# Optimization experiments

Measured on AMD Instinct MI355X. Metric: run time of the kernel, lower is better.

## Reference

```python
import jax, jax.numpy as jnp
import numpy as np

N = 100000   # nodes
E = 1600000  # edges (before self-loops)
HIDDEN = 256
BN_EPS = 1e-5


def setup_inputs() -> dict:
    key = jax.random.key(0)
    ks = jax.random.split(key, 16)
    def lin(k, i, o):
        return jax.random.normal(k, (i, o), jnp.float32) / np.float32(np.sqrt(i))
    inp = {
        "x": jax.random.normal(ks[0], (N, 21), jnp.float32),
        "edge_index": jax.random.randint(ks[1], (2, E), 0, N),
        # GCNConv weights (stored [in, out]) + biases
        "W1": lin(ks[2], 21, HIDDEN), "b1": jnp.zeros((HIDDEN,), jnp.float32),
        "W2": lin(ks[3], HIDDEN, 112), "b2": jnp.zeros((112,), jnp.float32),
        # dense MLP
        "lin2_w": lin(ks[4], 112, 256), "lin2_b": jnp.zeros((256,), jnp.float32),
        "lin3_w": lin(ks[5], 256, 100), "lin3_b": jnp.zeros((100,), jnp.float32),
        "lin4_w": lin(ks[6], 100, 1),   "lin4_b": jnp.zeros((1,), jnp.float32),
        # batchnorm affine params
        "g1": jnp.ones((112,), jnp.float32), "be1": jnp.zeros((112,), jnp.float32),
        "g2": jnp.ones((256,), jnp.float32), "be2": jnp.zeros((256,), jnp.float32),
        "g3": jnp.ones((100,), jnp.float32), "be3": jnp.zeros((100,), jnp.float32),
    }
    return inp


def _gcn_conv(x, W, b, src, dst, n):
    # PyG GCNConv: h = xW; out_i = sum_j norm_ij * h_j (+ bias), sym-normalized w/ self-loops
    h = x @ W                                              # [N, C]
    deg = jax.ops.segment_sum(jnp.ones(src.shape, h.dtype), dst, num_segments=n)
    dinv = jnp.where(deg > 0, jax.lax.rsqrt(deg), 0.0)
    norm = dinv[src] * dinv[dst]                            # [E']
    out = jax.ops.segment_sum(h[src] * norm[:, None], dst, num_segments=n)
    return out + b


def _bn(x, g, b):
    # train-mode batchnorm: biased batch variance
    m = jnp.mean(x, axis=0)
    v = jnp.mean(jnp.square(x - m), axis=0)
    return (x - m) * jax.lax.rsqrt(v + BN_EPS) * g + b


def reference(x, edge_index, W1, b1, W2, b2, lin2_w, lin2_b, lin3_w, lin3_b,
              lin4_w, lin4_b, g1, be1, g2, be2, g3, be3):
    n = x.shape[0]
    loops = jnp.arange(n, dtype=edge_index.dtype)
    src = jnp.concatenate([edge_index[0], loops])
    dst = jnp.concatenate([edge_index[1], loops])
    h = jax.nn.relu(_gcn_conv(x, W1, b1, src, dst, n))
    h = _gcn_conv(h, W2, b2, src, dst, n)
    h = jax.nn.relu(_bn(h, g1, be1))
    # dropout: identity (eval / deterministic)
    h = jax.nn.relu(_bn(h @ lin2_w + lin2_b, g2, be2))
    h = jax.nn.relu(_bn(h @ lin3_w + lin3_b, g3, be3))
    return h @ lin4_w + lin4_b
```

## Files before the change

kernel.cpp:

```cpp
#include <hip/hip_runtime.h>

#define N_NODES 100000
#define N_EDGES 1600000

typedef _Float16 f16x8 __attribute__((ext_vector_type(8)));
typedef _Float16 f16x4 __attribute__((ext_vector_type(4)));
typedef float fx4 __attribute__((ext_vector_type(4)));

#define NREP 16
#define NBUCK 196
#define CHUNK 8192
#define BCAP 12288

__global__ __launch_bounds__(256) void k_bin(const int* __restrict__ ei,
                                             unsigned* __restrict__ binned,
                                             int* __restrict__ gcount) {
  __shared__ unsigned pr[CHUNK];
  __shared__ unsigned srt[CHUNK];
  __shared__ unsigned char bk[CHUNK];
  __shared__ int hist[256], scanb[256], offs[256], bs[256], gb[256];
  const int t = threadIdx.x;
  const int e0 = blockIdx.x * CHUNK;
  const int n = min(CHUNK, N_EDGES - e0);
  hist[t] = 0;
  __syncthreads();
  for (int i = t; i < n; i += 256) {
    int src = ei[e0 + i], dst = ei[N_EDGES + e0 + i];
    int b = dst >> 9;
    pr[i] = ((unsigned)src << 9) | (unsigned)(dst & 511);
    bk[i] = (unsigned char)b;
    atomicAdd(&hist[b], 1);
  }
  __syncthreads();
  int v = hist[t];
  scanb[t] = v;
  __syncthreads();
  for (int off = 1; off < 256; off <<= 1) {
    int a = (t >= off) ? scanb[t - off] : 0;
    __syncthreads();
    scanb[t] += a;
    __syncthreads();
  }
  offs[t] = scanb[t] - v;
  bs[t] = scanb[t] - v;
  __syncthreads();
  for (int i = t; i < n; i += 256) {
    int b = bk[i];
    int p = atomicAdd(&offs[b], 1);
    srt[p] = pr[i];
  }
  if (t < NBUCK && v > 0) gb[t] = atomicAdd(&gcount[t], v);
  __syncthreads();
  int wave = t >> 6, lane = t & 63;
  for (int b = wave; b < NBUCK; b += 4) {
    int c = hist[b];
    if (c == 0) continue;
    int ls = bs[b], base = gb[b];
    unsigned* dstp = binned + (size_t)b * BCAP + base;
    for (int i = lane; i < c; i += 64) dstp[i] = srt[ls + i];
  }
}

__global__ void k_bscan(const int* __restrict__ gcount, int* __restrict__ gbase) {
  __shared__ int s[256];
  int t = threadIdx.x;
  int v = (t < NBUCK) ? gcount[t] : 0;
  s[t] = v;
  __syncthreads();
  for (int off = 1; off < 256; off <<= 1) {
    int a = (t >= off) ? s[t - off] : 0;
    __syncthreads();
    s[t] += a;
    __syncthreads();
  }
  if (t < NBUCK) gbase[t] = s[t] - v;
}

__global__ __launch_bounds__(256) void k_csr(const unsigned* __restrict__ binned,
                                             const int* __restrict__ gcount,
                                             const int* __restrict__ gbase,
                                             int* __restrict__ rowoff,
                                             int* __restrict__ cnt,
                                             float* __restrict__ dinv,
                                             int* __restrict__ csr) {
  __shared__ int hist[512], offs[512], ps[256];
  __shared__ unsigned srt[BCAP];
  const int b = blockIdx.x, t = threadIdx.x;
  const int n = min(gcount[b], BCAP);
  const int gb0 = gbase[b];
  const unsigned* bp = binned + (size_t)b * BCAP;
  hist[t] = 0;
  hist[t + 256] = 0;
  __syncthreads();
  for (int i = t; i < n; i += 256) atomicAdd(&hist[bp[i] & 511], 1);
  __syncthreads();
  int e0v = hist[2 * t], e1v = hist[2 * t + 1];
  ps[t] = e0v + e1v;
  __syncthreads();
  for (int off = 1; off < 256; off <<= 1) {
    int a = (t >= off) ? ps[t - off] : 0;
    __syncthreads();
    ps[t] += a;
    __syncthreads();
  }
  int excl = ps[t] - (e0v + e1v);
  offs[2 * t] = excl;
  offs[2 * t + 1] = excl + e0v;
  __syncthreads();
#pragma unroll
  for (int u = 0; u < 2; ++u) {
    int j = 2 * t + u;
    int nd = (b << 9) + j;
    if (nd < N_NODES) {
      int c = hist[j];
      cnt[nd] = c;
      dinv[nd] = rsqrtf((float)(c + 1));
      rowoff[nd] = gb0 + offs[j];
    }
  }
  __syncthreads();
  for (int i = t; i < n; i += 256) {
    unsigned p = bp[i];
    int d = p & 511;
    int pos = atomicAdd(&offs[d], 1);
    srt[pos] = p >> 9;
  }
  __syncthreads();
  for (int i = t; i < n; i += 256) csr[gb0 + i] = (int)srt[i];
}

__global__ void k_xpad(const float* __restrict__ x, const float* __restrict__ dinv,
                       _Float16* __restrict__ xs) {
  int idx = blockIdx.x * 256 + threadIdx.x;
  if (idx >= N_NODES * 24) return;
  int r = idx / 24, c = idx - r * 24;
  xs[idx] = (_Float16)((c < 21) ? x[r * 21 + c] * dinv[r] : 0.f);
}

__global__ __launch_bounds__(256) void k_aggx(
    const f16x8* __restrict__ xs3, const float* __restrict__ dinv,
    const int* __restrict__ rowoff, const int* __restrict__ cnt,
    const int* __restrict__ csr, float* __restrict__ aggx) {
  int lane = threadIdx.x & 63, wave = threadIdx.x >> 6;
  int j = lane / 3, c = lane - j * 3;
  if (j >= 21) return;
  int i = blockIdx.x * 84 + wave * 21 + j;
  if (i >= N_NODES) return;
  float di = dinv[i];
  int start = rowoff[i], len = cnt[i];
  f16x8 u = xs3[i * 3 + c];
  float a0[8], a1[8], a2[8], a3[8];
#pragma unroll
  for (int t = 0; t < 8; ++t) { a0[t] = (float)u[t]; a1[t] = a2[t] = a3[t] = 0.f; }
  int e = 0;
  for (; e + 3 < len; e += 4) {
    int s0 = csr[start + e], s1 = csr[start + e + 1];
    int s2 = csr[start + e + 2], s3 = csr[start + e + 3];
    f16x8 u0 = xs3[s0 * 3 + c];
    f16x8 u1 = xs3[s1 * 3 + c];
    f16x8 u2 = xs3[s2 * 3 + c];
    f16x8 u3 = xs3[s3 * 3 + c];
#pragma unroll
    for (int t = 0; t < 8; ++t) {
      a0[t] += (float)u0[t]; a1[t] += (float)u1[t];
      a2[t] += (float)u2[t]; a3[t] += (float)u3[t];
    }
  }
  for (; e < len; ++e) {
    int s0 = csr[start + e];
    f16x8 u0 = xs3[s0 * 3 + c];
#pragma unroll
    for (int t = 0; t < 8; ++t) a0[t] += (float)u0[t];
  }
  float4 r0, r1;
  r0.x = di * (a0[0] + a1[0] + a2[0] + a3[0]);
  r0.y = di * (a0[1] + a1[1] + a2[1] + a3[1]);
  r0.z = di * (a0[2] + a1[2] + a2[2] + a3[2]);
  r0.w = di * (a0[3] + a1[3] + a2[3] + a3[3]);
  r1.x = di * (a0[4] + a1[4] + a2[4] + a3[4]);
  r1.y = di * (a0[5] + a1[5] + a2[5] + a3[5]);
  r1.z = di * (a0[6] + a1[6] + a2[6] + a3[6]);
  r1.w = di * (a0[7] + a1[7] + a2[7] + a3[7]);
  *(float4*)(aggx + (size_t)i * 24 + c * 8) = r0;
  *(float4*)(aggx + (size_t)i * 24 + c * 8 + 4) = r1;
}

__global__ __launch_bounds__(256) void k_gemm1(const float4* __restrict__ aggx4,
                                               const float* __restrict__ W1,
                                               const float* __restrict__ b1,
                                               _Float16* __restrict__ h1) {
  __shared__ float As[32][24];
  int t = threadIdx.x;
  int base = blockIdx.x * 32;
  for (int idx = t; idx < 32 * 6; idx += 256) {
    int m = idx / 6, q = idx - m * 6;
    *(float4*)(&As[m][q * 4]) = aggx4[(base + m) * 6 + q];
  }
  float w[21];
#pragma unroll
  for (int k = 0; k < 21; ++k) w[k] = W1[k * 256 + t];
  float bias = b1[t];
  __syncthreads();
  for (int m = 0; m < 32; ++m) {
    float acc = bias;
#pragma unroll
    for (int k = 0; k < 21; ++k) acc = fmaf(As[m][k], w[k], acc);
    h1[(size_t)(base + m) * 256 + t] = (_Float16)fmaxf(acc, 0.f);
  }
}

template <int K, int KPAD, int NOUT, int NR>
__global__ void k_wcvt(const float* __restrict__ W, _Float16* __restrict__ Wh) {
  int idx = blockIdx.x * 256 + threadIdx.x;
  if (idx >= NR * KPAD) return;
  int n = idx / KPAD, k = idx % KPAD;
  float v = (n < NOUT && k < K) ? W[k * NOUT + n] : 0.f;
  Wh[idx] = (_Float16)v;
}

template <int K, int KPAD, int NT, int MT, int WR, int WC, int MINW,
          bool BN, bool STATS, bool F16IN, bool F16OUT>
__global__ __launch_bounds__(256, MINW) void k_mgemm(
    const void* __restrict__ Av, const _Float16* __restrict__ Wt,
    const float* __restrict__ bias, const float* __restrict__ bn_a,
    const float* __restrict__ bn_c, const float* __restrict__ rowscale,
    void* __restrict__ Cv, int NOUTr, float* __restrict__ sums,
    float* __restrict__ sqs) {
  constexpr int BM = WR * MT * 16;
  constexpr int NR = WC * NT * 16;
  constexpr int BKP = 40;
  constexpr int NC = KPAD / 32;
  constexpr int AIT = BM * 4 / 256;
  constexpr int ABYTES = BM * BKP * 2;
  constexpr int BBYTES = NR * BKP * 2;
  __shared__ __align__(16) char smem[ABYTES + BBYTES];
  _Float16* Ah = (_Float16*)smem;
  _Float16* Bh = (_Float16*)(smem + ABYTES);
  const float* A32 = (const float*)Av;
  const _Float16* A16 = (const _Float16*)Av;
  float* C = (float*)Cv;
  _Float16* C16 = (_Float16*)Cv;

  const int tid = threadIdx.x;
  const int lane = tid & 63, wave = tid >> 6;
  const int wr = wave % WR, wc = wave / WR;
  const int quad = lane >> 4, ln = lane & 15;
  const int rowbase = blockIdx.x * BM;

  fx4 acc[MT][NT];
#pragma unroll
  for (int mt = 0; mt < MT; ++mt)
#pragma unroll
    for (int j = 0; j < NT; ++j) acc[mt][j] = (fx4){0.f, 0.f, 0.f, 0.f};

  f16x8 pf16[AIT];
  fx4 pf32a[AIT], pf32b[AIT];

  auto loadA = [&](int kc) {
#pragma unroll
    for (int it = 0; it < AIT; ++it) {
      int idx = tid + it * 256;
      int m = idx >> 2, q = idx & 3;
      int gi = rowbase + m;
      int k = kc * 32 + q * 8;
      bool ok = (gi < N_NODES) && (k < K);
      if constexpr (F16IN) {
        f16x8 z;
#pragma unroll
        for (int t = 0; t < 8; ++t) z[t] = (_Float16)0;
        pf16[it] = ok ? *(const f16x8*)(A16 + (size_t)gi * K + k) : z;
      } else {
        if (ok) {
          pf32a[it] = *(const fx4*)(A32 + (size_t)gi * K + k);
          pf32b[it] = *(const fx4*)(A32 + (size_t)gi * K + k + 4);
        } else {
          pf32a[it] = (fx4){0.f, 0.f, 0.f, 0.f};
          pf32b[it] = (fx4){0.f, 0.f, 0.f, 0.f};
        }
      }
    }
  };

  auto writeA = [&](int kc) {
#pragma unroll
    for (int it = 0; it < AIT; ++it) {
      int idx = tid + it * 256;
      int m = idx >> 2, q = idx & 3;
      int k = kc * 32 + q * 8;
      float vv[8];
      if constexpr (F16IN) {
#pragma unroll
        for (int t = 0; t < 8; ++t) vv[t] = (float)pf16[it][t];
      } else {
#pragma unroll
        for (int t = 0; t < 4; ++t) { vv[t] = pf32a[it][t]; vv[t + 4] = pf32b[it][t]; }
      }
      if constexpr (BN) {
        if (k < K) {
          float4 a0 = *(const float4*)(bn_a + k);
          float4 a1 = *(const float4*)(bn_a + k + 4);
          float4 c0 = *(const float4*)(bn_c + k);
          float4 c1 = *(const float4*)(bn_c + k + 4);
          float av[8] = {a0.x, a0.y, a0.z, a0.w, a1.x, a1.y, a1.z, a1.w};
          float cv[8] = {c0.x, c0.y, c0.z, c0.w, c1.x, c1.y, c1.z, c1.w};
#pragma unroll
          for (int t = 0; t < 8; ++t) vv[t] = fmaxf(fmaf(vv[t], av[t], cv[t]), 0.f);
        }
      }
      f16x8 hv;
#pragma unroll
      for (int t = 0; t < 8; ++t) hv[t] = (_Float16)vv[t];
      *(f16x8*)(Ah + m * BKP + q * 8) = hv;
    }
  };

  loadA(0);
  for (int kc = 0; kc < NC; ++kc) {
    __syncthreads();
    writeA(kc);
    for (int idx = tid; idx < NR * 4; idx += 256) {
      int n = idx >> 2, p = idx & 3;
      *(f16x8*)(Bh + n * BKP + p * 8) =
          *(const f16x8*)(Wt + n * KPAD + kc * 32 + p * 8);
    }
    __syncthreads();
    if (kc + 1 < NC) loadA(kc + 1);
    f16x8 nf[MT];
#pragma unroll
    for (int mt = 0; mt < MT; ++mt) {
      int r = (wr * MT + mt) * 16 + ln;
      nf[mt] = *(const f16x8*)(Ah + r * BKP + quad * 8);
    }
#pragma unroll
    for (int j = 0; j < NT; ++j) {
      int n = (wc * NT + j) * 16 + ln;
      f16x8 wh = *(const f16x8*)(Bh + n * BKP + quad * 8);
#pragma unroll
      for (int mt = 0; mt < MT; ++mt)
        acc[mt][j] = __builtin_amdgcn_mfma_f32_16x16x32_f16(wh, nf[mt], acc[mt][j], 0, 0, 0);
    }
  }

  float* s_s = (float*)smem;
  float* s_q = s_s + NR;
  __syncthreads();
  if constexpr (STATS) {
    for (int c = tid; c < 2 * NR; c += 256) s_s[c] = 0.f;
    __syncthreads();
  }
  float rs[MT];
#pragma unroll
  for (int mt = 0; mt < MT; ++mt) {
    int nd = rowbase + (wr * MT + mt) * 16 + ln;
    rs[mt] = (rowscale != nullptr && nd < N_NODES) ? rowscale[nd] : 1.f;
  }
#pragma unroll
  for (int j = 0; j < NT; ++j) {
    int ch0 = (wc * NT + j) * 16 + quad * 4;
    bool cv = ch0 < NOUTr;
    float4 b4 = make_float4(0.f, 0.f, 0.f, 0.f);
    if (cv && bias != nullptr) b4 = *(const float4*)(bias + ch0);
    float sc[4] = {0.f, 0.f, 0.f, 0.f}, sq[4] = {0.f, 0.f, 0.f, 0.f};
#pragma unroll
    for (int mt = 0; mt < MT; ++mt) {
      int nd = rowbase + (wr * MT + mt) * 16 + ln;
      if (nd < N_NODES && cv) {
        float v0 = (acc[mt][j][0] + b4.x) * rs[mt];
        float v1 = (acc[mt][j][1] + b4.y) * rs[mt];
        float v2 = (acc[mt][j][2] + b4.z) * rs[mt];
        float v3 = (acc[mt][j][3] + b4.w) * rs[mt];
        if constexpr (F16OUT) {
          f16x4 o = {(_Float16)v0, (_Float16)v1, (_Float16)v2, (_Float16)v3};
          *(f16x4*)(C16 + (size_t)nd * NOUTr + ch0) = o;
        } else {
          float4 o = make_float4(v0, v1, v2, v3);
          *(float4*)(C + (size_t)nd * NOUTr + ch0) = o;
        }
        if constexpr (STATS) {
          sc[0] += v0; sq[0] = fmaf(v0, v0, sq[0]);
          sc[1] += v1; sq[1] = fmaf(v1, v1, sq[1]);
          sc[2] += v2; sq[2] = fmaf(v2, v2, sq[2]);
          sc[3] += v3; sq[3] = fmaf(v3, v3, sq[3]);
        }
      }
    }
    if constexpr (STATS) {
      if (cv) {
#pragma unroll
        for (int r = 0; r < 4; ++r) {
          float s = sc[r], q = sq[r];
          s += __shfl_xor(s, 1); q += __shfl_xor(q, 1);
          s += __shfl_xor(s, 2); q += __shfl_xor(q, 2);
          s += __shfl_xor(s, 4); q += __shfl_xor(q, 4);
          s += __shfl_xor(s, 8); q += __shfl_xor(q, 8);
          if (ln == 0) {
            atomicAdd(&s_s[ch0 + r], s);
            atomicAdd(&s_q[ch0 + r], q);
          }
        }
      }
    }
  }
  if constexpr (STATS) {
    __syncthreads();
    int rep = (blockIdx.x & (NREP - 1));
    for (int c = tid; c < NR; c += 256) {
      if (c < NOUTr) {
        atomicAdd(&sums[rep * NOUTr + c], s_s[c]);
        atomicAdd(&sqs[rep * NOUTr + c], s_q[c]);
      }
    }
  }
}

__global__ __launch_bounds__(256) void k_agg2(
    const f16x8* __restrict__ t2s8, const float* __restrict__ dinv,
    const int* __restrict__ rowoff, const int* __restrict__ cnt,
    const int* __restrict__ csr, const float* __restrict__ b2,
    _Float16* __restrict__ g2) {
  int lane = threadIdx.x & 63, wave = threadIdx.x >> 6;
  int j = lane / 14, c = lane - j * 14;
  if (j >= 4) return;
  int i = blockIdx.x * 16 + wave * 4 + j;
  float di = dinv[i];
  int start = rowoff[i], len = cnt[i];
  f16x8 u = t2s8[i * 14 + c];
  float a0[8], a1[8], a2[8], a3[8];
#pragma unroll
  for (int t = 0; t < 8; ++t) { a0[t] = (float)u[t]; a1[t] = a2[t] = a3[t] = 0.f; }
  int e = 0;
  for (; e + 3 < len; e += 4) {
    int s0 = csr[start + e], s1 = csr[start + e + 1];
    int s2 = csr[start + e + 2], s3 = csr[start + e + 3];
    f16x8 u0 = t2s8[s0 * 14 + c];
    f16x8 u1 = t2s8[s1 * 14 + c];
    f16x8 u2 = t2s8[s2 * 14 + c];
    f16x8 u3 = t2s8[s3 * 14 + c];
#pragma unroll
    for (int t = 0; t < 8; ++t) {
      a0[t] += (float)u0[t]; a1[t] += (float)u1[t];
      a2[t] += (float)u2[t]; a3[t] += (float)u3[t];
    }
  }
  for (; e < len; ++e) {
    int s0 = csr[start + e];
    f16x8 u0 = t2s8[s0 * 14 + c];
#pragma unroll
    for (int t = 0; t < 8; ++t) a0[t] += (float)u0[t];
  }
  float4 blo = *(const float4*)(b2 + c * 8);
  float4 bhi = *(const float4*)(b2 + c * 8 + 4);
  float bb[8] = {blo.x, blo.y, blo.z, blo.w, bhi.x, bhi.y, bhi.z, bhi.w};
  f16x8 o;
#pragma unroll
  for (int t = 0; t < 8; ++t)
    o[t] = (_Float16)fmaf(di, a0[t] + a1[t] + a2[t] + a3[t], bb[t]);
  *(f16x8*)(g2 + (size_t)i * 112 + c * 8) = o;
}

template <int C>
__global__ void k_colstats16(const _Float16* __restrict__ X, float* __restrict__ sums,
                             float* __restrict__ sqs) {
  int c = threadIdx.x;
  if (c >= C) return;
  int chunk = (N_NODES + gridDim.x - 1) / gridDim.x;
  int i0 = blockIdx.x * chunk;
  int i1 = min(N_NODES, i0 + chunk);
  float s = 0.f, q = 0.f;
  for (int i = i0; i < i1; ++i) {
    float v = (float)X[(size_t)i * C + c];
    s += v;
    q = fmaf(v, v, q);
  }
  int rep = (blockIdx.x & (NREP - 1));
  atomicAdd(&sums[rep * C + c], s);
  atomicAdd(&sqs[rep * C + c], q);
}

template <int C>
__global__ void k_bnfinal(const float* __restrict__ sums, const float* __restrict__ sqs,
                          const float* __restrict__ gamma, const float* __restrict__ beta,
                          float* __restrict__ bn_a, float* __restrict__ bn_c) {
  int c = threadIdx.x;
  if (c >= C) return;
  float s = 0.f, q = 0.f;
#pragma unroll
  for (int r = 0; r < NREP; ++r) {
    s += sums[r * C + c];
    q += sqs[r * C + c];
  }
  const float inv_n = 1.0f / (float)N_NODES;
  float mean = s * inv_n;
  float var = fmaxf(q * inv_n - mean * mean, 0.f);
  float rstd = 1.0f / sqrtf(var + 1e-5f);
  float a = gamma[c] * rstd;
  bn_a[c] = a;
  bn_c[c] = beta[c] - mean * a;
}

__global__ void k_final(const float* __restrict__ h4, const float* __restrict__ bn_a,
                        const float* __restrict__ bn_c, const float* __restrict__ w4,
                        const float* __restrict__ b4, float* __restrict__ out) {
  int lane = threadIdx.x & 63;
  int i = blockIdx.x * 4 + (threadIdx.x >> 6);
  float acc = fmaxf(fmaf(h4[(size_t)i * 100 + lane], bn_a[lane], bn_c[lane]), 0.f) * w4[lane];
  if (lane < 36) {
    int k = lane + 64;
    acc += fmaxf(fmaf(h4[(size_t)i * 100 + k], bn_a[k], bn_c[k]), 0.f) * w4[k];
  }
#pragma unroll
  for (int off = 32; off >= 1; off >>= 1) acc += __shfl_down(acc, off);
  if (lane == 0) out[i] = acc + b4[0];
}

extern "C" void kernel_launch(void* const* d_in, const int* in_sizes, int n_in,
                              void* d_out, int out_size, void* d_ws, size_t ws_size,
                              hipStream_t stream) {
  const float* x   = (const float*)d_in[0];
  const int*   ei  = (const int*)d_in[1];
  const float* W1  = (const float*)d_in[2];
  const float* b1  = (const float*)d_in[3];
  const float* W2  = (const float*)d_in[4];
  const float* b2  = (const float*)d_in[5];
  const float* l2w = (const float*)d_in[6];
  const float* l2b = (const float*)d_in[7];
  const float* l3w = (const float*)d_in[8];
  const float* l3b = (const float*)d_in[9];
  const float* l4w = (const float*)d_in[10];
  const float* l4b = (const float*)d_in[11];
  const float* g1  = (const float*)d_in[12];
  const float* be1 = (const float*)d_in[13];
  const float* g2w = (const float*)d_in[14];
  const float* be2 = (const float*)d_in[15];
  const float* g3  = (const float*)d_in[16];
  const float* be3 = (const float*)d_in[17];
  float* out = (float*)d_out;

  char* base = (char*)d_ws;
  size_t off = 0;
  auto alloc = [&](size_t bytes) -> char* {
    char* p = base + off;
    off = (off + bytes + 255) & ~(size_t)255;
    return p;
  };
  int*   cnt    = (int*)alloc((size_t)N_NODES * 4);
  int*   rowoff = (int*)alloc((size_t)N_NODES * 4);
  float* dinv   = (float*)alloc((size_t)N_NODES * 4);
  int*   csr    = (int*)alloc((size_t)N_EDGES * 4);
  unsigned* binned = (unsigned*)alloc((size_t)NBUCK * BCAP * 4);
  int*   gcount = (int*)alloc(NBUCK * 4);
  int*   gbase  = (int*)alloc(NBUCK * 4);
  float* stats  = (float*)alloc((size_t)NREP * 960 * 4);
  float* bnco   = (float*)alloc(960 * 4);
  _Float16* xs  = (_Float16*)alloc((size_t)N_NODES * 24 * 2);
  float* aggx   = (float*)alloc((size_t)N_NODES * 24 * 4);
  _Float16* h1  = (_Float16*)alloc((size_t)N_NODES * 256 * 2);
  _Float16* t2s = (_Float16*)alloc((size_t)N_NODES * 112 * 2);
  _Float16* g2h = (_Float16*)alloc((size_t)N_NODES * 112 * 2);
  float* h4     = (float*)alloc((size_t)N_NODES * 112 * 4);
  _Float16* wt2 = (_Float16*)alloc(112 * 256 * 2);
  _Float16* wt3 = (_Float16*)alloc(256 * 128 * 2);
  _Float16* wt4 = (_Float16*)alloc(112 * 256 * 2);

  float* sums1 = stats;
  float* sqs1  = sums1 + NREP * 112;
  float* sums2 = sqs1 + NREP * 112;
  float* sqs2  = sums2 + NREP * 256;
  float* sums3 = sqs2 + NREP * 256;
  float* sqs3  = sums3 + NREP * 112;
  float* bn_a1 = bnco + 0,   *bn_c1 = bnco + 112;
  float* bn_a2 = bnco + 224, *bn_c2 = bnco + 480;
  float* bn_a3 = bnco + 736, *bn_c3 = bnco + 848;

  hipMemsetAsync(gcount, 0, NBUCK * 4, stream);
  hipMemsetAsync(stats, 0, (size_t)NREP * 960 * 4, stream);

  k_bin<<<NBUCK, 256, 0, stream>>>(ei, binned, gcount);
  k_bscan<<<1, 256, 0, stream>>>(gcount, gbase);
  k_csr<<<NBUCK, 256, 0, stream>>>(binned, gcount, gbase, rowoff, cnt, dinv, csr);

  k_wcvt<256, 256, 112, 112><<<112, 256, 0, stream>>>(W2, wt2);
  k_wcvt<112, 128, 256, 256><<<128, 256, 0, stream>>>(l2w, wt3);
  k_wcvt<256, 256, 100, 112><<<112, 256, 0, stream>>>(l3w, wt4);

  k_xpad<<<(N_NODES * 24 + 255) / 256, 256, 0, stream>>>(x, dinv, xs);
  k_aggx<<<(N_NODES + 83) / 84, 256, 0, stream>>>((const f16x8*)xs, dinv, rowoff,
                                                  cnt, csr, aggx);
  k_gemm1<<<3125, 256, 0, stream>>>((const float4*)aggx, W1, b1, h1);

  k_mgemm<256, 256, 7, 2, 4, 1, 4, false, false, true, true><<<782, 256, 0, stream>>>(
      h1, wt2, nullptr, nullptr, nullptr, dinv, t2s, 112, nullptr, nullptr);
  k_agg2<<<6250, 256, 0, stream>>>((const f16x8*)t2s, dinv, rowoff, cnt, csr, b2,
                                   g2h);

  k_colstats16<112><<<1600, 128, 0, stream>>>(g2h, sums1, sqs1);
  k_bnfinal<112><<<1, 128, 0, stream>>>(sums1, sqs1, g1, be1, bn_a1, bn_c1);

  k_mgemm<112, 128, 8, 2, 2, 2, 4, true, true, true, true><<<1563, 256, 0, stream>>>(
      g2h, wt3, l2b, bn_a1, bn_c1, nullptr, h1, 256, sums2, sqs2);
  k_bnfinal<256><<<1, 256, 0, stream>>>(sums2, sqs2, g2w, be2, bn_a2, bn_c2);

  k_mgemm<256, 256, 7, 2, 4, 1, 4, true, true, true, false><<<782, 256, 0, stream>>>(
      h1, wt4, l3b, bn_a2, bn_c2, nullptr, h4, 100, sums3, sqs3);
  k_bnfinal<100><<<1, 128, 0, stream>>>(sums3, sqs3, g3, be3, bn_a3, bn_c3);

  k_final<<<25000, 256, 0, stream>>>(h4, bn_a3, bn_c3, l4w, l4b, out);
}
```

Baseline: 414.8 us.

## Split layer-2 features into two 64-wide halves for cache-friendly aggregation

The 112-channel layer-2 GEMM output is now written as two separate 56-channel arrays, each padded to a 64-element (128-byte) row. Aggregation runs as two passes, one per half, with 8 lanes per node instead of 14. Each pass gathers from a 12.8 MB table rather than 22 MB, which should give better cache hit rates and aligned 128-byte row fetches. The cost is a second pass over the CSR indices, an extra kernel launch, and one idle lane in eight for the padding.

After: 411.4 us. About the same (-0.8%).

```diff
diff --git a/kernel.cpp b/kernel.cpp
--- a/kernel.cpp
+++ b/kernel.cpp
@@ -219,13 +219,13 @@
 }
 
 template <int K, int KPAD, int NT, int MT, int WR, int WC, int MINW,
-          bool BN, bool STATS, bool F16IN, bool F16OUT>
+          bool BN, bool STATS, bool F16IN, bool F16OUT, bool SPLIT>
 __global__ __launch_bounds__(256, MINW) void k_mgemm(
     const void* __restrict__ Av, const _Float16* __restrict__ Wt,
     const float* __restrict__ bias, const float* __restrict__ bn_a,
     const float* __restrict__ bn_c, const float* __restrict__ rowscale,
-    void* __restrict__ Cv, int NOUTr, float* __restrict__ sums,
-    float* __restrict__ sqs) {
+    void* __restrict__ Cv, void* __restrict__ Cv2, int NOUTr,
+    float* __restrict__ sums, float* __restrict__ sqs) {
   constexpr int BM = WR * MT * 16;
   constexpr int NR = WC * NT * 16;
   constexpr int BKP = 40;
@@ -240,6 +240,7 @@
   const _Float16* A16 = (const _Float16*)Av;
   float* C = (float*)Cv;
   _Float16* C16 = (_Float16*)Cv;
+  _Float16* C16b = (_Float16*)Cv2;
 
   const int tid = threadIdx.x;
   const int lane = tid & 63, wave = tid >> 6;
@@ -371,7 +372,14 @@
         float v3 = (acc[mt][j][3] + b4.w) * rs[mt];
         if constexpr (F16OUT) {
           f16x4 o = {(_Float16)v0, (_Float16)v1, (_Float16)v2, (_Float16)v3};
-          *(f16x4*)(C16 + (size_t)nd * NOUTr + ch0) = o;
+          if constexpr (SPLIT) {
+            _Float16* dp = (ch0 < 56)
+                ? C16 + (size_t)nd * 64 + ch0
+                : C16b + (size_t)nd * 64 + (ch0 - 56);
+            *(f16x4*)dp = o;
+          } else {
+            *(f16x4*)(C16 + (size_t)nd * NOUTr + ch0) = o;
+          }
         } else {
           float4 o = make_float4(v0, v1, v2, v3);
           *(float4*)(C + (size_t)nd * NOUTr + ch0) = o;
@@ -414,17 +422,16 @@
 }
 
 __global__ __launch_bounds__(256) void k_agg2(
-    const f16x8* __restrict__ t2s8, const float* __restrict__ dinv,
+    const f16x8* __restrict__ t2x8, const float* __restrict__ dinv,
     const int* __restrict__ rowoff, const int* __restrict__ cnt,
     const int* __restrict__ csr, const float* __restrict__ b2,
-    _Float16* __restrict__ g2) {
+    _Float16* __restrict__ g2, int off) {
   int lane = threadIdx.x & 63, wave = threadIdx.x >> 6;
-  int j = lane / 14, c = lane - j * 14;
-  if (j >= 4) return;
-  int i = blockIdx.x * 16 + wave * 4 + j;
+  int j = lane >> 3, c = lane & 7;
+  int i = blockIdx.x * 32 + wave * 8 + j;
   float di = dinv[i];
   int start = rowoff[i], len = cnt[i];
-  f16x8 u = t2s8[i * 14 + c];
+  f16x8 u = t2x8[i * 8 + c];
   float a0[8], a1[8], a2[8], a3[8];
 #pragma unroll
   for (int t = 0; t < 8; ++t) { a0[t] = (float)u[t]; a1[t] = a2[t] = a3[t] = 0.f; }
@@ -432,10 +439,10 @@
   for (; e + 3 < len; e += 4) {
     int s0 = csr[start + e], s1 = csr[start + e + 1];
     int s2 = csr[start + e + 2], s3 = csr[start + e + 3];
-    f16x8 u0 = t2s8[s0 * 14 + c];
-    f16x8 u1 = t2s8[s1 * 14 + c];
-    f16x8 u2 = t2s8[s2 * 14 + c];
-    f16x8 u3 = t2s8[s3 * 14 + c];
+    f16x8 u0 = t2x8[s0 * 8 + c];
+    f16x8 u1 = t2x8[s1 * 8 + c];
+    f16x8 u2 = t2x8[s2 * 8 + c];
+    f16x8 u3 = t2x8[s3 * 8 + c];
 #pragma unroll
     for (int t = 0; t < 8; ++t) {
       a0[t] += (float)u0[t]; a1[t] += (float)u1[t];
@@ -444,18 +451,20 @@
   }
   for (; e < len; ++e) {
     int s0 = csr[start + e];
-    f16x8 u0 = t2s8[s0 * 14 + c];
+    f16x8 u0 = t2x8[s0 * 8 + c];
 #pragma unroll
     for (int t = 0; t < 8; ++t) a0[t] += (float)u0[t];
   }
-  float4 blo = *(const float4*)(b2 + c * 8);
-  float4 bhi = *(const float4*)(b2 + c * 8 + 4);
-  float bb[8] = {blo.x, blo.y, blo.z, blo.w, bhi.x, bhi.y, bhi.z, bhi.w};
-  f16x8 o;
-#pragma unroll
-  for (int t = 0; t < 8; ++t)
-    o[t] = (_Float16)fmaf(di, a0[t] + a1[t] + a2[t] + a3[t], bb[t]);
-  *(f16x8*)(g2 + (size_t)i * 112 + c * 8) = o;
+  if (c < 7) {
+    float4 blo = *(const float4*)(b2 + off + c * 8);
+    float4 bhi = *(const float4*)(b2 + off + c * 8 + 4);
+    float bb[8] = {blo.x, blo.y, blo.z, blo.w, bhi.x, bhi.y, bhi.z, bhi.w};
+    f16x8 o;
+#pragma unroll
+    for (int t = 0; t < 8; ++t)
+      o[t] = (_Float16)fmaf(di, a0[t] + a1[t] + a2[t] + a3[t], bb[t]);
+    *(f16x8*)(g2 + (size_t)i * 112 + off + c * 8) = o;
+  }
 }
 
 template <int C>
@@ -555,7 +564,8 @@
   _Float16* xs  = (_Float16*)alloc((size_t)N_NODES * 24 * 2);
   float* aggx   = (float*)alloc((size_t)N_NODES * 24 * 4);
   _Float16* h1  = (_Float16*)alloc((size_t)N_NODES * 256 * 2);
-  _Float16* t2s = (_Float16*)alloc((size_t)N_NODES * 112 * 2);
+  _Float16* t2a = (_Float16*)alloc((size_t)N_NODES * 64 * 2);
+  _Float16* t2b = (_Float16*)alloc((size_t)N_NODES * 64 * 2);
   _Float16* g2h = (_Float16*)alloc((size_t)N_NODES * 112 * 2);
   float* h4     = (float*)alloc((size_t)N_NODES * 112 * 4);
   _Float16* wt2 = (_Float16*)alloc(112 * 256 * 2);
@@ -588,20 +598,25 @@
                                                   cnt, csr, aggx);
   k_gemm1<<<3125, 256, 0, stream>>>((const float4*)aggx, W1, b1, h1);
 
-  k_mgemm<256, 256, 7, 2, 4, 1, 4, false, false, true, true><<<782, 256, 0, stream>>>(
-      h1, wt2, nullptr, nullptr, nullptr, dinv, t2s, 112, nullptr, nullptr);
-  k_agg2<<<6250, 256, 0, stream>>>((const f16x8*)t2s, dinv, rowoff, cnt, csr, b2,
-                                   g2h);
+  k_mgemm<256, 256, 7, 2, 4, 1, 4, false, false, true, true, true>
+      <<<782, 256, 0, stream>>>(h1, wt2, nullptr, nullptr, nullptr, dinv,
+                                t2a, t2b, 112, nullptr, nullptr);
+  k_agg2<<<3125, 256, 0, stream>>>((const f16x8*)t2a, dinv, rowoff, cnt, csr, b2,
+                                   g2h, 0);
+  k_agg2<<<3125, 256, 0, stream>>>((const f16x8*)t2b, dinv, rowoff, cnt, csr, b2,
+                                   g2h, 56);
 
   k_colstats16<112><<<1600, 128, 0, stream>>>(g2h, sums1, sqs1);
   k_bnfinal<112><<<1, 128, 0, stream>>>(sums1, sqs1, g1, be1, bn_a1, bn_c1);
 
-  k_mgemm<112, 128, 8, 2, 2, 2, 4, true, true, true, true><<<1563, 256, 0, stream>>>(
-      g2h, wt3, l2b, bn_a1, bn_c1, nullptr, h1, 256, sums2, sqs2);
+  k_mgemm<112, 128, 8, 2, 2, 2, 4, true, true, true, true, false>
+      <<<1563, 256, 0, stream>>>(g2h, wt3, l2b, bn_a1, bn_c1, nullptr,
+                                 h1, nullptr, 256, sums2, sqs2);
   k_bnfinal<256><<<1, 256, 0, stream>>>(sums2, sqs2, g2w, be2, bn_a2, bn_c2);
 
-  k_mgemm<256, 256, 7, 2, 4, 1, 4, true, true, true, false><<<782, 256, 0, stream>>>(
-      h1, wt4, l3b, bn_a2, bn_c2, nullptr, h4, 100, sums3, sqs3);
+  k_mgemm<256, 256, 7, 2, 4, 1, 4, true, true, true, false, false>
+      <<<782, 256, 0, stream>>>(h1, wt4, l3b, bn_a2, bn_c2, nullptr,
+                                h4, nullptr, 100, sums3, sqs3);
   k_bnfinal<100><<<1, 128, 0, stream>>>(sums3, sqs3, g3, be3, bn_a3, bn_c3);
 
   k_final<<<25000, 256, 0, stream>>>(h4, bn_a3, bn_c3, l4w, l4b, out);
```
